# Optimization experiments

Measured on AMD Instinct MI355X. Metric: run time of the kernel, lower is better.

The kernel has to match this reference:

```python
import jax, jax.numpy as jnp
import numpy as np

NUM_SEGMENTS = 4096  # number of graphs in the batch


def setup_inputs() -> dict:
    key = jax.random.key(0)
    k1, k2, k3, k4, k5, k6 = jax.random.split(key, 6)
    N, H = 1048576, 128
    x = jax.random.normal(k1, (N, H), dtype=jnp.float32)
    batch = jnp.sort(jax.random.randint(k2, (N,), 0, NUM_SEGMENTS, dtype=jnp.int64))
    # Linear params, PyTorch layout: W [out, in], b [out]
    W1 = jax.random.normal(k3, (2 * H, H), dtype=jnp.float32) * (1.0 / np.sqrt(H))
    b1 = jax.random.normal(k4, (2 * H,), dtype=jnp.float32) * 0.01
    W2 = jax.random.normal(k5, (H, 2 * H), dtype=jnp.float32) * (1.0 / np.sqrt(2 * H))
    b2 = jax.random.normal(k6, (H,), dtype=jnp.float32) * 0.01
    return {"x": x, "batch": batch, "W1": W1, "b1": b1, "W2": W2, "b2": b2}


def reference(x, batch, W1, b1, W2, b2):
    # phi(x) = tanh(fc1(x))  -> [N, 2H]
    phi_x = jnp.tanh(jnp.einsum('nh,oh->no', x, W1) + b1)
    # scatter-sum pooling per graph -> [G, 2H]
    sum_x = jax.ops.segment_sum(phi_x, batch, num_segments=NUM_SEGMENTS)
    # fc2 -> [G, H]; .squeeze() is a no-op for these shapes
    y = jnp.einsum('go,ho->gh', sum_x, W2) + b2
    return jnp.squeeze(y)
```

## Files before the change

### kernel.cpp

```cpp
#include <hip/hip_runtime.h>
#include <hip/hip_bf16.h>

#define NTOT 1048576
#define NSEG 4096
#define HDIM 128
#define ODIM 256
#define BN   64
#define GRID1 1024
#define TPB  (NTOT / (BN * GRID1))

typedef __attribute__((ext_vector_type(8))) short bf16x8;
typedef __attribute__((ext_vector_type(4))) float f32x4;
typedef __attribute__((ext_vector_type(4))) unsigned int u32x4;

typedef const __attribute__((address_space(1))) unsigned int* gp_t;
typedef __attribute__((address_space(3))) unsigned int* lp_t;

__device__ __forceinline__ unsigned short f32_to_bf16_rne(float f) {
    unsigned int u = __builtin_bit_cast(unsigned int, f);
    return (unsigned short)((u + 0x7fffu + ((u >> 16) & 1u)) >> 16);
}
__device__ __forceinline__ unsigned int pk_bf16(float lo, float hi) {
    return ((unsigned int)f32_to_bf16_rne(hi) << 16) | f32_to_bf16_rne(lo);
}

__global__ void zero_convert(const float* __restrict__ W1, unsigned int* __restrict__ W1b,
                             float* __restrict__ sumx) {
    int gid = blockIdx.x * 256 + threadIdx.x;
    sumx[gid] = 0.0f;
    if (gid < (ODIM * HDIM / 2)) {
        float2 v = *(const float2*)(W1 + 2 * gid);
        W1b[gid] = pk_bf16(v.x, v.y);
    }
}

__global__ __launch_bounds__(256, 2)
void stage1(const float* __restrict__ x, const int* __restrict__ batch,
            const unsigned short* __restrict__ W1b, const float* __restrict__ b1,
            float* __restrict__ sumx) {
    __shared__ __align__(16) float xbuf[2][BN * HDIM];
    __shared__ int segAll[TPB * BN];

    const int t    = threadIdx.x;
    const int lane = t & 63;
    const int wv   = t >> 6;
    const int l15  = lane & 15;
    const int lhi  = (lane >> 4) & 3;

    const bool is64 = (batch[NTOT - 1] == 0);
    const long r0 = (long)blockIdx.x * (TPB * BN);

    for (int i = t; i < TPB * BN; i += 256) {
        long idx = r0 + i;
        segAll[i] = batch[is64 ? 2 * idx : idx];
    }

    bf16x8 bfr[4][4];
    #pragma unroll
    for (int nf = 0; nf < 4; ++nf)
        #pragma unroll
        for (int ks = 0; ks < 4; ++ks)
            bfr[nf][ks] = *(const bf16x8*)(W1b + (wv * 64 + nf * 16 + l15) * HDIM + ks * 32 + lhi * 8);

    float bias[4];
    #pragma unroll
    for (int nf = 0; nf < 4; ++nf) bias[nf] = b1[wv * 64 + nf * 16 + l15];

    int doff[8];
    #pragma unroll
    for (int j = 0; j < 8; ++j) {
        int b   = wv * 8 + j;
        int row = ((b >> 1) & 3) * 16 + l15;
        int c4  = (b >> 3) * 8 + lhi * 2 + (b & 1);
        doff[j] = row * 512 + c4 * 16;
    }

    const char* xb = (const char*)x + (size_t)r0 * (HDIM * 4);

    #pragma unroll
    for (int j = 0; j < 8; ++j)
        __builtin_amdgcn_global_load_lds((gp_t)(xb + doff[j]),
                                         (lp_t)(&xbuf[0][(wv * 8 + j) * 64 * 4]), 16, 0, 0);
    __syncthreads();

    for (int g = 0; g < TPB; ++g) {
        const int nb = g & 1;

        if (g + 1 < TPB) {
            const char* src = xb + (size_t)(g + 1) * (BN * HDIM * 4);
            #pragma unroll
            for (int j = 0; j < 8; ++j)
                __builtin_amdgcn_global_load_lds((gp_t)(src + doff[j]),
                                                 (lp_t)(&xbuf[nb ^ 1][(wv * 8 + j) * 64 * 4]), 16, 0, 0);
        }

        f32x4 acc[4][4];
        #pragma unroll
        for (int nf = 0; nf < 4; ++nf) {
            float bb = bias[nf];
            #pragma unroll
            for (int mf = 0; mf < 4; ++mf)
                acc[mf][nf] = (f32x4){bb, bb, bb, bb};
        }
        const f32x4* fb = (const f32x4*)&xbuf[nb][0];
        #pragma unroll
        for (int ks = 0; ks < 4; ++ks) {
            #pragma unroll
            for (int mf = 0; mf < 4; ++mf) {
                f32x4 u = fb[(ks * 8 + mf * 2) * 64 + lane];
                f32x4 v = fb[(ks * 8 + mf * 2 + 1) * 64 + lane];
                u32x4 w;
                w.x = pk_bf16(u.x, u.y); w.y = pk_bf16(u.z, u.w);
                w.z = pk_bf16(v.x, v.y); w.w = pk_bf16(v.z, v.w);
                bf16x8 af = __builtin_bit_cast(bf16x8, w);
                #pragma unroll
                for (int nf = 0; nf < 4; ++nf)
                    acc[mf][nf] = __builtin_amdgcn_mfma_f32_16x16x32_bf16(af, bfr[nf][ks], acc[mf][nf], 0, 0, 0);
            }
        }

        #pragma unroll
        for (int mf = 0; mf < 4; ++mf)
            #pragma unroll
            for (int nf = 0; nf < 4; ++nf)
                #pragma unroll
                for (int r = 0; r < 4; ++r) {
                    float e = exp2f(acc[mf][nf][r] * 2.885390081777927f);
                    acc[mf][nf][r] = 1.0f - 2.0f * __builtin_amdgcn_rcpf(1.0f + e);
                }

        const int* segc = &segAll[g * 64];
        unsigned long long bmask;
        {
            int s_here = segc[lane];
            int s_prev = (lane > 0) ? segc[lane - 1] : s_here;
            bmask = __ballot(s_here != s_prev);
        }
        int start = 0;
        unsigned long long rem = bmask;
        for (;;) {
            const int end = rem ? (int)__builtin_ctzll(rem) : BN;
            const int sid = segc[start];
            float p0 = 0.f, p1 = 0.f, p2 = 0.f, p3 = 0.f;
            #pragma unroll
            for (int mf = 0; mf < 4; ++mf)
                #pragma unroll
                for (int r = 0; r < 4; ++r) {
                    int row = mf * 16 + lhi * 4 + r;
                    float w = ((unsigned)(row - start) < (unsigned)(end - start)) ? 1.0f : 0.0f;
                    p0 = fmaf(w, acc[mf][0][r], p0);
                    p1 = fmaf(w, acc[mf][1][r], p1);
                    p2 = fmaf(w, acc[mf][2][r], p2);
                    p3 = fmaf(w, acc[mf][3][r], p3);
                }
            p0 += __shfl_xor(p0, 16); p0 += __shfl_xor(p0, 32);
            p1 += __shfl_xor(p1, 16); p1 += __shfl_xor(p1, 32);
            p2 += __shfl_xor(p2, 16); p2 += __shfl_xor(p2, 32);
            p3 += __shfl_xor(p3, 16); p3 += __shfl_xor(p3, 32);
            if (lhi == 0) {
                float* base = sumx + (long)sid * ODIM + wv * 64 + l15;
                atomicAdd(base +  0, p0);
                atomicAdd(base + 16, p1);
                atomicAdd(base + 32, p2);
                atomicAdd(base + 48, p3);
            }
            if (rem == 0) break;
            start = end;
            rem &= rem - 1;
        }

        __syncthreads();
    }
}

__global__ __launch_bounds__(256)
void stage2(const float* __restrict__ sumx, const float* __restrict__ W2,
            const float* __restrict__ b2, float* __restrict__ y) {
    __shared__ float sx[16 * 256];
    const int t = threadIdx.x;
    const long g0 = (long)blockIdx.x * 16;
    #pragma unroll
    for (int i = 0; i < 16; ++i)
        sx[i * 256 + t] = sumx[(g0 + i) * 256 + t];
    __syncthreads();
    const int h = t & 127;
    const int gl0 = (t >> 7) * 8;
    float acc[8] = {0, 0, 0, 0, 0, 0, 0, 0};
    const float* w = W2 + h * 256;
    for (int o4 = 0; o4 < 64; ++o4) {
        float4 wvv = *(const float4*)(w + o4 * 4);
        #pragma unroll
        for (int gl = 0; gl < 8; ++gl) {
            const float* sr = &sx[(gl0 + gl) * 256 + o4 * 4];
            acc[gl] += sr[0] * wvv.x + sr[1] * wvv.y + sr[2] * wvv.z + sr[3] * wvv.w;
        }
    }
    float bb = b2[h];
    #pragma unroll
    for (int gl = 0; gl < 8; ++gl)
        y[(g0 + gl0 + gl) * 128 + h] = acc[gl] + bb;
}

extern "C" void kernel_launch(void* const* d_in, const int* in_sizes, int n_in,
                              void* d_out, int out_size, void* d_ws, size_t ws_size,
                              hipStream_t stream) {
    const float* x   = (const float*)d_in[0];
    const int* batch = (const int*)d_in[1];
    const float* W1  = (const float*)d_in[2];
    const float* b1  = (const float*)d_in[3];
    const float* W2  = (const float*)d_in[4];
    const float* b2  = (const float*)d_in[5];
    float* y = (float*)d_out;

    float* sumx = (float*)d_ws;
    unsigned short* W1b = (unsigned short*)((char*)d_ws + (size_t)NSEG * ODIM * 4);

    zero_convert<<<dim3(NSEG), dim3(256), 0, stream>>>(W1, (unsigned int*)W1b, sumx);
    stage1<<<dim3(GRID1), dim3(256), 0, stream>>>(x, batch, W1b, b1, sumx);
    stage2<<<dim3(NSEG / 16), dim3(256), 0, stream>>>(sumx, W2, b2, y);
}
```

Before: 233.0 us.

## Convert x tile to bf16 once per block into swizzled LDS, single fp32 buffer

Each x tile is now converted from fp32 to bf16 once by the whole block and written into an XOR-swizzled bf16 LDS buffer. Previously each of the four waves converted the full tile itself. Conversion uses the hardware v_cvt_pk_bf16_f32 instruction instead of manual round-to-nearest bit arithmetic. The fp32 staging buffer drops from double to single buffering to cut LDS use, and occupancy is raised to 3 blocks per CU. In exchange, there is an extra barrier per tile, and the next tile's load is only issued after conversion, which reduces overlap.

```diff
diff --git a/kernel.cpp b/kernel.cpp
--- a/kernel.cpp
+++ b/kernel.cpp
@@ -11,17 +11,15 @@
 
 typedef __attribute__((ext_vector_type(8))) short bf16x8;
 typedef __attribute__((ext_vector_type(4))) float f32x4;
-typedef __attribute__((ext_vector_type(4))) unsigned int u32x4;
+typedef __attribute__((ext_vector_type(2))) unsigned int u32x2;
 
 typedef const __attribute__((address_space(1))) unsigned int* gp_t;
 typedef __attribute__((address_space(3))) unsigned int* lp_t;
 
-__device__ __forceinline__ unsigned short f32_to_bf16_rne(float f) {
-    unsigned int u = __builtin_bit_cast(unsigned int, f);
-    return (unsigned short)((u + 0x7fffu + ((u >> 16) & 1u)) >> 16);
-}
-__device__ __forceinline__ unsigned int pk_bf16(float lo, float hi) {
-    return ((unsigned int)f32_to_bf16_rne(hi) << 16) | f32_to_bf16_rne(lo);
+__device__ __forceinline__ unsigned int cvt_pk(float lo, float hi) {
+    unsigned int r;
+    asm("v_cvt_pk_bf16_f32 %0, %1, %2" : "=v"(r) : "v"(lo), "v"(hi));
+    return r;
 }
 
 __global__ void zero_convert(const float* __restrict__ W1, unsigned int* __restrict__ W1b,
@@ -30,15 +28,16 @@
     sumx[gid] = 0.0f;
     if (gid < (ODIM * HDIM / 2)) {
         float2 v = *(const float2*)(W1 + 2 * gid);
-        W1b[gid] = pk_bf16(v.x, v.y);
-    }
-}
-
-__global__ __launch_bounds__(256, 2)
+        W1b[gid] = cvt_pk(v.x, v.y);
+    }
+}
+
+__global__ __launch_bounds__(256, 3)
 void stage1(const float* __restrict__ x, const int* __restrict__ batch,
             const unsigned short* __restrict__ W1b, const float* __restrict__ b1,
             float* __restrict__ sumx) {
-    __shared__ __align__(16) float xbuf[2][BN * HDIM];
+    __shared__ __align__(16) float fbuf[BN * HDIM];
+    __shared__ __align__(16) unsigned char bbuf[BN * 256];
     __shared__ int segAll[TPB * BN];
 
     const int t    = threadIdx.x;
@@ -49,70 +48,69 @@
 
     const bool is64 = (batch[NTOT - 1] == 0);
     const long r0 = (long)blockIdx.x * (TPB * BN);
+    const char* xb = (const char*)(x + r0 * HDIM);
+
+    #pragma unroll
+    for (int j = 0; j < 8; ++j) {
+        const int c0 = j * 256 + wv * 64;
+        __builtin_amdgcn_global_load_lds((gp_t)(xb + (size_t)(c0 + lane) * 16),
+                                         (lp_t)(fbuf + c0 * 4), 16, 0, 0);
+    }
 
     for (int i = t; i < TPB * BN; i += 256) {
         long idx = r0 + i;
         segAll[i] = batch[is64 ? 2 * idx : idx];
     }
-
     bf16x8 bfr[4][4];
     #pragma unroll
     for (int nf = 0; nf < 4; ++nf)
         #pragma unroll
         for (int ks = 0; ks < 4; ++ks)
             bfr[nf][ks] = *(const bf16x8*)(W1b + (wv * 64 + nf * 16 + l15) * HDIM + ks * 32 + lhi * 8);
-
     float bias[4];
     #pragma unroll
     for (int nf = 0; nf < 4; ++nf) bias[nf] = b1[wv * 64 + nf * 16 + l15];
 
-    int doff[8];
-    #pragma unroll
-    for (int j = 0; j < 8; ++j) {
-        int b   = wv * 8 + j;
-        int row = ((b >> 1) & 3) * 16 + l15;
-        int c4  = (b >> 3) * 8 + lhi * 2 + (b & 1);
-        doff[j] = row * 512 + c4 * 16;
-    }
-
-    const char* xb = (const char*)x + (size_t)r0 * (HDIM * 4);
-
-    #pragma unroll
-    for (int j = 0; j < 8; ++j)
-        __builtin_amdgcn_global_load_lds((gp_t)(xb + doff[j]),
-                                         (lp_t)(&xbuf[0][(wv * 8 + j) * 64 * 4]), 16, 0, 0);
     __syncthreads();
 
     for (int g = 0; g < TPB; ++g) {
-        const int nb = g & 1;
+        #pragma unroll
+        for (int j = 0; j < 8; ++j) {
+            const int c = j * 256 + t;
+            f32x4 v = ((const f32x4*)fbuf)[c];
+            u32x2 p;
+            p.x = cvt_pk(v.x, v.y);
+            p.y = cvt_pk(v.z, v.w);
+            const int row = c >> 5, c4 = c & 31;
+            *(u32x2*)(bbuf + row * 256 + ((c4 * 8) ^ ((row & 7) << 4))) = p;
+        }
+        __syncthreads();
 
         if (g + 1 < TPB) {
             const char* src = xb + (size_t)(g + 1) * (BN * HDIM * 4);
             #pragma unroll
-            for (int j = 0; j < 8; ++j)
-                __builtin_amdgcn_global_load_lds((gp_t)(src + doff[j]),
-                                                 (lp_t)(&xbuf[nb ^ 1][(wv * 8 + j) * 64 * 4]), 16, 0, 0);
+            for (int j = 0; j < 8; ++j) {
+                const int c0 = j * 256 + wv * 64;
+                __builtin_amdgcn_global_load_lds((gp_t)(src + (size_t)(c0 + lane) * 16),
+                                                 (lp_t)(fbuf + c0 * 4), 16, 0, 0);
+            }
         }
 
         f32x4 acc[4][4];
         #pragma unroll
         for (int nf = 0; nf < 4; ++nf) {
-            float bb = bias[nf];
+            const float bb = bias[nf];
             #pragma unroll
             for (int mf = 0; mf < 4; ++mf)
                 acc[mf][nf] = (f32x4){bb, bb, bb, bb};
         }
-        const f32x4* fb = (const f32x4*)&xbuf[nb][0];
         #pragma unroll
         for (int ks = 0; ks < 4; ++ks) {
+            const int k0 = ks * 32 + lhi * 8;
             #pragma unroll
             for (int mf = 0; mf < 4; ++mf) {
-                f32x4 u = fb[(ks * 8 + mf * 2) * 64 + lane];
-                f32x4 v = fb[(ks * 8 + mf * 2 + 1) * 64 + lane];
-                u32x4 w;
-                w.x = pk_bf16(u.x, u.y); w.y = pk_bf16(u.z, u.w);
-                w.z = pk_bf16(v.x, v.y); w.w = pk_bf16(v.z, v.w);
-                bf16x8 af = __builtin_bit_cast(bf16x8, w);
+                const int m = mf * 16 + l15;
+                bf16x8 af = *(const bf16x8*)(bbuf + m * 256 + ((k0 * 2) ^ ((m & 7) << 4)));
                 #pragma unroll
                 for (int nf = 0; nf < 4; ++nf)
                     acc[mf][nf] = __builtin_amdgcn_mfma_f32_16x16x32_bf16(af, bfr[nf][ks], acc[mf][nf], 0, 0, 0);
@@ -129,7 +127,7 @@
                     acc[mf][nf][r] = 1.0f - 2.0f * __builtin_amdgcn_rcpf(1.0f + e);
                 }
 
-        const int* segc = &segAll[g * 64];
+        const int* segc = &segAll[g * BN];
         unsigned long long bmask;
         {
             int s_here = segc[lane];
```

After: 388.6 us. 1.67x slower.
